# Kernel optimization log

Measured on AMD Instinct MI355X. Metric: run time of the kernel, lower is better.

## Reference

```python
import jax, jax.numpy as jnp
import numpy as np

B, S, D = 4, 4096, 1024

def setup_inputs() -> dict:
    key = jax.random.key(0)
    ks = jax.random.split(key, 8)
    scale = 1.0 / np.sqrt(D)
    return {
        "inputs": jax.random.normal(ks[0], (B, S, D), dtype=jnp.float32),
        "context": jax.random.normal(ks[1], (B, S, D), dtype=jnp.float32),
        "Wq": jax.random.normal(ks[2], (D, D), dtype=jnp.float32) * scale,
        "bq": jnp.zeros((D,), dtype=jnp.float32),
        "Wk": jax.random.normal(ks[3], (D, D), dtype=jnp.float32) * scale,
        "bk": jnp.zeros((D,), dtype=jnp.float32),
        "Wv": jax.random.normal(ks[4], (D, D), dtype=jnp.float32) * scale,
        "bv": jnp.zeros((D,), dtype=jnp.float32),
        "Wo": jax.random.normal(ks[5], (D, D), dtype=jnp.float32) * scale,
        "bo": jnp.zeros((D,), dtype=jnp.float32),
    }

def reference(inputs, context, Wq, bq, Wk, bk, Wv, bv, Wo, bo):
    phi = lambda x: jax.nn.elu(x) + 1.0
    q_phi = phi(jnp.einsum("bsd,de->bse", inputs, Wq) + bq)   # [B,S,D]
    k_phi = phi(jnp.einsum("bsd,de->bse", context, Wk) + bk)  # [B,S,D]
    v = jnp.einsum("bsd,de->bse", context, Wv) + bv           # [B,S,D]
    kv = jnp.einsum("bsd,bse->bde", k_phi, v)                 # [B,D,D]
    k_sum = jnp.sum(k_phi, axis=1)                            # [B,D]
    z = 1.0 / (jnp.einsum("bsd,bd->bs", q_phi, k_sum)[..., None] + 1e-6)  # [B,S,1]
    out = jnp.einsum("bsd,bde->bse", q_phi, kv) * z           # [B,S,D]
    return jnp.einsum("bsd,de->bse", out, Wo) + bo + inputs
```

## Files before the change

kernel.cpp:

```cpp
#include <hip/hip_runtime.h>


typedef __bf16 bf16x8 __attribute__((ext_vector_type(8)));
typedef __bf16 bf16x4 __attribute__((ext_vector_type(4)));
typedef float  f32x4  __attribute__((ext_vector_type(4)));

#define GLOBAL_AS __attribute__((address_space(1)))
#define LDS_AS    __attribute__((address_space(3)))

#define SS 4096
#define DD 1024

__device__ __forceinline__ __bf16 f2bf(float f) {
  union { float f; unsigned u; } a; a.f = f;
  unsigned r = a.u + 0x7FFFu + ((a.u >> 16) & 1u);
  union { unsigned short s; __bf16 b; } o; o.s = (unsigned short)(r >> 16);
  return o.b;
}

__device__ __forceinline__ void async_load16(const void* g, void* l) {
  __builtin_amdgcn_global_load_lds((const GLOBAL_AS void*)g, (LDS_AS void*)l, 16, 0, 0);
}


#define LA0 0
#define LA1 16384
#define LB0 32768
#define LB1 49152

#define VMW(n)  asm volatile("s_waitcnt vmcnt(" #n ")" ::: "memory")
#define SBAR()  asm volatile("s_barrier" ::: "memory")

#define STG_A(BASE, mh, kt) do {                                              \
    async_load16(Aa + (long)((mh)*64 + t6) * K + (kt)*64 + gc8,               \
                 smem + (BASE) + (mh)*8192 + tid*8);                          \
    async_load16(Aa + (long)(128 + (mh)*64 + t6) * K + (kt)*64 + gc8,         \
                 smem + (BASE) + (mh)*8192 + 4096 + tid*8);                   \
  } while (0)

#define STG_B(BASE, nh, kt) do {                                              \
    async_load16(Bb + (long)(tA*64 + (nh)*32 + t5) * K + (kt)*64 + gc8,       \
                 smem + (BASE) + (nh)*8192 + tid*8);                          \
    async_load16(Bb + (long)(128 + tA*64 + (nh)*32 + t5) * K + (kt)*64 + gc8, \
                 smem + (BASE) + (nh)*8192 + 4096 + tid*8);                   \
  } while (0)

#define RD_A(dst, AB, mh)                                                     \
    _Pragma("unroll") for (int rr = 0; rr < 4; ++rr) {                        \
      const int o = (AB) + (mh)*8192 + rr*1024 + aoff;                        \
      dst[rr][0] = *(const bf16x8*)(smem + o);                                \
      dst[rr][1] = *(const bf16x8*)(smem + (o ^ 32));                         \
    }

#define RD_B(dst, BB, nh)                                                     \
    _Pragma("unroll") for (int nn = 0; nn < 2; ++nn) {                        \
      const int o = (BB) + (nh)*8192 + nn*1024 + boff;                        \
      dst[nn][0] = *(const bf16x8*)(smem + o);                                \
      dst[nn][1] = *(const bf16x8*)(smem + (o ^ 32));                         \
    }

#define MM(mh, nh, af, bf)                                                    \
    __builtin_amdgcn_s_setprio(1);                                            \
    _Pragma("unroll") for (int rr = 0; rr < 4; ++rr)                          \
    _Pragma("unroll") for (int nn = 0; nn < 2; ++nn) {                        \
      acc[(mh)*4+rr][(nh)*2+nn] = __builtin_amdgcn_mfma_f32_16x16x32_bf16(    \
          af[rr][0], bf[nn][0], acc[(mh)*4+rr][(nh)*2+nn], 0, 0, 0);          \
      acc[(mh)*4+rr][(nh)*2+nn] = __builtin_amdgcn_mfma_f32_16x16x32_bf16(    \
          af[rr][1], bf[nn][1], acc[(mh)*4+rr][(nh)*2+nn], 0, 0, 0);          \
    }                                                                         \
    __builtin_amdgcn_s_setprio(0)

#define PH(VM, STG, RDS, MMM) do {                                            \
    VM; STG; RDS;                                                             \
    SBAR();                                                                   \
    MMM;                                                                      \
  } while (0)

template<int MODE>
__global__ __launch_bounds__(512, 2)
void gemm256(const __bf16* __restrict__ Ag, const __bf16* __restrict__ Bg,
             void* __restrict__ Cg, void* __restrict__ Cg2,
             int N, int K, long sB,
             const float* __restrict__ bias, const float* __restrict__ bias2,
             const float* __restrict__ zvec, const float* __restrict__ resid)
{
  union SMem {
    __bf16 st[65536];
    __bf16 T[256 * 136];
  };
  __shared__ SMem sm;
  __bf16* smem = sm.st;

  int bx = blockIdx.x, by = blockIdx.y;
  {
    const int gx = gridDim.x, gy = gridDim.y;
    if ((gy & 7) == 0) {
      const int f = by * gx + bx;
      const int j = f & 7;
      const int u = f >> 3;
      bx = u % gx;
      by = j * (gy >> 3) + u / gx;
    }
  }

  const int tid  = threadIdx.x;
  const int lane = tid & 63, wave = tid >> 6;
  const int wm   = wave >> 2, wn = wave & 3;
  const int ln   = lane & 15, quad = lane >> 4;
  const int t6   = tid >> 3, tA = t6 >> 5, t5 = t6 & 31;
  const int gc8  = ((tid & 7) ^ (t6 & 7)) * 8;
  const int pco  = (quad ^ (ln & 7)) * 8;
  const int aoff = (wm * 64 + ln) * 64 + pco;
  const int boff = (wn * 32 + ln) * 64 + pco;

  const long m0  = (long)by * 256;
  const int  n0g = bx * 256;
  const __bf16* Aa = Ag + m0 * K;
  const __bf16* Bb = Bg + (long)bx * 256 * K +
                     ((MODE == 8) ? (long)(m0 >> 12) * sB : 0);

  f32x4 acc[8][4];
  const f32x4 zero = {0.f, 0.f, 0.f, 0.f};
#pragma unroll
  for (int i = 0; i < 8; i++)
#pragma unroll
    for (int j = 0; j < 4; j++) acc[i][j] = zero;

  STG_A(LA0, 0, 0); STG_B(LB0, 0, 0);
  STG_A(LA0, 1, 0); STG_B(LB0, 1, 0);
  STG_A(LA1, 0, 1); STG_B(LB1, 0, 1);
  VMW(8);
  SBAR();

  const int niter = K >> 7;
#pragma unroll 1
  for (int i = 0; i < niter - 1; ++i) {
    const int kb = i * 2;
    bf16x8 a[4][2], b[2][2], b1[2][2];
    PH(VMW(4), STG_A(LA1,1,kb+1), RD_A(a,LA0,0) RD_B(b,LB0,0), MM(0,0,a,b));
    PH(      , STG_B(LB1,1,kb+1), RD_B(b1,LB0,1),              MM(0,1,a,b1));
    PH(      , STG_A(LA0,0,kb+2), RD_A(a,LA0,1),               MM(1,1,a,b1));
    PH(VMW(6), STG_B(LB0,0,kb+2), ,                            MM(1,0,a,b));
    PH(VMW(4), STG_A(LA0,1,kb+2), RD_A(a,LA1,0) RD_B(b,LB1,0), MM(0,0,a,b));
    PH(      , STG_B(LB0,1,kb+2), RD_B(b1,LB1,1),              MM(0,1,a,b1));
    PH(      , STG_A(LA1,0,kb+3), RD_A(a,LA1,1),               MM(1,1,a,b1));
    PH(VMW(6), STG_B(LB1,0,kb+3), ,                            MM(1,0,a,b));
  }
  {
    const int kb = (niter - 1) * 2;
    bf16x8 a[4][2], b[2][2], b1[2][2];
    PH(VMW(4), STG_A(LA1,1,kb+1), RD_A(a,LA0,0) RD_B(b,LB0,0), MM(0,0,a,b));
    PH(      , STG_B(LB1,1,kb+1), RD_B(b1,LB0,1),              MM(0,1,a,b1));
    PH(      , ,                  RD_A(a,LA0,1),               MM(1,1,a,b1));
    PH(VMW(0), ,                  ,                            MM(1,0,a,b));
    PH(      , ,                  RD_A(a,LA1,0) RD_B(b,LB1,0), MM(0,0,a,b));
    PH(      , ,                  RD_B(b1,LB1,1),              MM(0,1,a,b1));
    PH(      , ,                  RD_A(a,LA1,1),               MM(1,1,a,b1));
    PH(      , ,                  ,                            MM(1,0,a,b));
    SBAR();
  }

  if (MODE == 6) {
    const bool isK = (n0g < 1024);
    const float* bb = isK ? bias : bias2;
    const int nb = isK ? n0g : (n0g - 1024);
    const int b = (int)(m0 >> 12);
    const long s_in = m0 & 4095;
    __bf16* dst = (__bf16*)(isK ? Cg : Cg2) + (long)b * DD * SS;
#pragma unroll
    for (int h = 0; h < 2; ++h) {
      if (wm == h) {
#pragma unroll
        for (int mf = 0; mf < 8; ++mf)
#pragma unroll
          for (int nf = 0; nf < 4; ++nf) {
            const int nl = wn * 64 + nf * 16 + ln;
            const int sl0 = mf * 16 + quad * 4;
            const float bv = bb[nb + nl];
            bf16x4 pk;
#pragma unroll
            for (int r = 0; r < 4; ++r) {
              float x = acc[mf][nf][r] + bv;
              if (isK) x = (x > 0.f) ? (x + 1.f) : __expf(x);
              pk[r] = f2bf(x);
            }
            *(bf16x4*)(sm.T + nl * 136 + sl0) = pk;
          }
      }
      __syncthreads();
#pragma unroll
      for (int p2 = 0; p2 < 8; ++p2) {
        const int row = (tid >> 4) + p2 * 32;
        const int c   = (tid & 15) * 8;
        bf16x8 vv = *(const bf16x8*)(sm.T + row * 136 + c);
        *(bf16x8*)&dst[(long)(nb + row) * SS + s_in + h * 128 + c] = vv;
      }
      __syncthreads();
    }
    return;
  }

#pragma unroll
  for (int mf = 0; mf < 8; ++mf)
#pragma unroll
    for (int nf = 0; nf < 4; ++nf)
#pragma unroll
      for (int r = 0; r < 4; ++r) {
        const long gm = m0 + wm * 128 + mf * 16 + quad * 4 + r;
        const int  gn = n0g + wn * 64 + nf * 16 + ln;
        float x = acc[mf][nf][r];
        if (MODE == 0) {
          x += bias[gn];
          x = (x > 0.f) ? (x + 1.f) : __expf(x);
          ((__bf16*)Cg)[gm * (long)N + gn] = f2bf(x);
        } else {
          x = x * zvec[gm] + bias[gn];
          ((float*)Cg)[gm * (long)N + gn] = x + resid[gm * (long)N + gn];
        }
      }
}

#undef PH
#undef MM
#undef RD_A
#undef RD_B
#undef STG_A
#undef STG_B

template<int MODE>
__global__ __launch_bounds__(256)
void gemm_bt(const __bf16* __restrict__ Ag, const __bf16* __restrict__ Bg,
             void* __restrict__ Cg, void* __restrict__ Cg2,
             int N, int K, long sA, long sB, long sC,
             const float* __restrict__ bias, const float* __restrict__ bias2,
             const float* __restrict__ zvec,
             const float* __restrict__ resid)
{
  union SMem {
    struct { __bf16 As[128 * 64]; __bf16 Bs[128 * 64]; } s;
    __bf16 T[128 * 136];
  };
  __shared__ SMem sm;

  int bx = blockIdx.x, by = blockIdx.y;
  {
    const int gx = gridDim.x, gy = gridDim.y;
    if ((gy & 7) == 0) {
      const int f = by * gx + bx;
      const int j = f & 7;
      const int u = f >> 3;
      bx = u % gx;
      by = j * (gy >> 3) + u / gx;
    }
  }
  int bz = blockIdx.z;
  int k0beg = 0, k0end = K;
  if (MODE == 5) {
    const int split = bz & 3;
    bz >>= 2;
    k0beg = split * (K >> 2);
    k0end = k0beg + (K >> 2);
  }

  const int tid = threadIdx.x;
  const long m0 = (long)by * 128;
  const __bf16* A = Ag + m0 * K + bz * sA;
  const __bf16* B = Bg + (long)bx * 128 * K + bz * sB;

  const int srow = tid >> 3;
  const int gcc8 = ((tid & 7) ^ (srow & 7)) * 8;

  const int lane = tid & 63;
  const int wave = tid >> 6;
  const int wm   = (wave >> 1) * 64;
  const int wn   = (wave & 1) * 64;
  const int ln   = lane & 15;
  const int quad = lane >> 4;
  const int rk   = ln & 7;

  f32x4 acc[4][4];
  const f32x4 zero = {0.f, 0.f, 0.f, 0.f};
#pragma unroll
  for (int i = 0; i < 4; i++)
#pragma unroll
    for (int j = 0; j < 4; j++) acc[i][j] = zero;

  for (int k0 = k0beg; k0 < k0end; k0 += 64) {
#pragma unroll
    for (int p = 0; p < 4; p++) {
      async_load16(A + (long)(p * 32 + srow) * K + k0 + gcc8, sm.s.As + p * 2048 + tid * 8);
      async_load16(B + (long)(p * 32 + srow) * K + k0 + gcc8, sm.s.Bs + p * 2048 + tid * 8);
    }
    __syncthreads();

#pragma unroll
    for (int ksub = 0; ksub < 2; ksub++) {
      const int cc = (ksub * 4 + quad) ^ rk;
      bf16x8 af[4], bfr[4];
#pragma unroll
      for (int i = 0; i < 4; i++)
        af[i] = *(const bf16x8*)(sm.s.As + (wm + i * 16 + ln) * 64 + cc * 8);
#pragma unroll
      for (int j = 0; j < 4; j++)
        bfr[j] = *(const bf16x8*)(sm.s.Bs + (wn + j * 16 + ln) * 64 + cc * 8);
#pragma unroll
      for (int i = 0; i < 4; i++)
#pragma unroll
        for (int j = 0; j < 4; j++)
          acc[i][j] = __builtin_amdgcn_mfma_f32_16x16x32_bf16(af[i], bfr[j], acc[i][j], 0, 0, 0);
    }
    __syncthreads();
  }

  const int n0g = bx * 128;
#pragma unroll
  for (int i = 0; i < 4; i++) {
#pragma unroll
    for (int j = 0; j < 4; j++) {
#pragma unroll
      for (int r = 0; r < 4; r++) {
        const int lrow = wm + i * 16 + quad * 4 + r;
        const int lcol = wn + j * 16 + ln;
        const long gm  = m0 + lrow;
        const int  gn  = n0g + lcol;
        float x = acc[i][j][r];
        if (MODE == 5) {
          __hip_atomic_fetch_add(&((float*)Cg)[(long)bz * sC + gm * (long)N + gn],
                                 x, __ATOMIC_RELAXED, __HIP_MEMORY_SCOPE_AGENT);
        } else if (MODE == 7) {
          ((__bf16*)Cg)[(long)bz * sC + gm * (long)N + gn] = f2bf(x);
        }
      }
    }
  }
}

__global__ __launch_bounds__(256)
void cvt_f32_bf16(const float* __restrict__ x, __bf16* __restrict__ y, long n)
{
  long i = ((long)blockIdx.x * 256 + threadIdx.x) * 4;
  if (i < n) {
    float4 v = *(const float4*)(x + i);
    bf16x4 o;
    o[0] = f2bf(v.x); o[1] = f2bf(v.y); o[2] = f2bf(v.z); o[3] = f2bf(v.w);
    *(bf16x4*)(y + i) = o;
  }
}

__global__ __launch_bounds__(256)
void wtrans(const float* W0, const float* W1, const float* W2, const float* W3,
            __bf16* O0, __bf16* O1, __bf16* O2, __bf16* O3, int Dd)
{
  __shared__ __bf16 t[64][72];
  const float* W = (blockIdx.z == 0) ? W0 : (blockIdx.z == 1) ? W1 : (blockIdx.z == 2) ? W2 : W3;
  __bf16*      O = (blockIdx.z == 0) ? O0 : (blockIdx.z == 1) ? O1 : (blockIdx.z == 2) ? O2 : O3;
  const int r0 = blockIdx.y * 64, c0 = blockIdx.x * 64;
  const int tid = threadIdx.x;
  const int lr4 = tid >> 4, lc4 = (tid & 15) * 4;
#pragma unroll
  for (int it = 0; it < 4; it++) {
    const int row = lr4 + it * 16;
    float4 v = *(const float4*)&W[(long)(r0 + row) * Dd + c0 + lc4];
    t[row][lc4 + 0] = f2bf(v.x);
    t[row][lc4 + 1] = f2bf(v.y);
    t[row][lc4 + 2] = f2bf(v.z);
    t[row][lc4 + 3] = f2bf(v.w);
  }
  __syncthreads();
  const int lr8 = tid >> 3, lc8 = (tid & 7) * 8;
#pragma unroll
  for (int it = 0; it < 2; it++) {
    const int orow = lr8 + it * 32;
    bf16x8 vb;
#pragma unroll
    for (int j = 0; j < 8; j++) vb[j] = t[lc8 + j][orow];
    *(bf16x8*)&O[(long)(c0 + orow) * Dd + r0 + lc8] = vb;
  }
}

__global__ __launch_bounds__(256)
void ksum_k(const __bf16* __restrict__ kphiT, float* __restrict__ ksum, int S)
{
  const long row = blockIdx.x;
  const __bf16* p = kphiT + row * (long)S;
  const int tid = threadIdx.x;
  float s = 0.f;
  for (int j = tid * 8; j < S; j += 256 * 8) {
    bf16x8 v = *(const bf16x8*)&p[j];
#pragma unroll
    for (int e = 0; e < 8; e++) s += (float)v[e];
  }
  __shared__ float red[256];
  red[tid] = s; __syncthreads();
  for (int off = 128; off > 0; off >>= 1) {
    if (tid < off) red[tid] += red[tid + off];
    __syncthreads();
  }
  if (tid == 0) ksum[row] = red[0];
}

__global__ __launch_bounds__(256)
void zden_k(const __bf16* __restrict__ qphi, const float* __restrict__ ksum,
            float* __restrict__ z, int Dd, int S)
{
  const long row = blockIdx.x;
  const int  b   = (int)(row / S);
  const __bf16* q = qphi + row * (long)Dd;
  const float* ks = ksum + (long)b * Dd;
  const int tid = threadIdx.x;
  const int i = tid * 4;
  bf16x4 qv = *(const bf16x4*)&q[i];
  float4 kv4 = *(const float4*)&ks[i];
  float s = (float)qv[0] * kv4.x + (float)qv[1] * kv4.y +
            (float)qv[2] * kv4.z + (float)qv[3] * kv4.w;
  __shared__ float red[256];
  red[tid] = s; __syncthreads();
  for (int off = 128; off > 0; off >>= 1) {
    if (tid < off) red[tid] += red[tid + off];
    __syncthreads();
  }
  if (tid == 0) z[row] = 1.f / (red[0] + 1e-6f);
}

extern "C" void kernel_launch(void* const* d_in, const int* in_sizes, int n_in,
                              void* d_out, int out_size, void* d_ws, size_t ws_size,
                              hipStream_t stream)
{
  const float* inputs  = (const float*)d_in[0];
  const float* context = (const float*)d_in[1];
  const float* Wq = (const float*)d_in[2];
  const float* bq = (const float*)d_in[3];
  const float* Wk = (const float*)d_in[4];
  const float* bk = (const float*)d_in[5];
  const float* Wv = (const float*)d_in[6];
  const float* bv = (const float*)d_in[7];
  const float* Wo = (const float*)d_in[8];
  const float* bo = (const float*)d_in[9];
  float* out = (float*)d_out;

  const int Bn = 4;
  const long NSD = (long)Bn * SS * DD;
  const long MB = 1L << 20;

  char* ws = (char*)d_ws;
  __bf16* xbf   = (__bf16*)(ws + 0 * MB);
  __bf16* cbf   = (__bf16*)(ws + 32 * MB);
  __bf16* qphi  = (__bf16*)(ws + 64 * MB);
  __bf16* kphiT = (__bf16*)(ws + 96 * MB);
  __bf16* vT    = (__bf16*)(ws + 128 * MB);
  float*  kvf   = (float*)(ws + 160 * MB);
  __bf16* kvbf  = (__bf16*)(ws + 176 * MB);
  __bf16* M2T   = (__bf16*)(ws + 184 * MB);
  __bf16* WqT   = (__bf16*)(ws + 192 * MB);
  __bf16* WkT   = (__bf16*)(ws + 194 * MB);
  __bf16* WvT   = (__bf16*)(ws + 196 * MB);
  __bf16* WoT   = (__bf16*)(ws + 198 * MB);
  float*  ksum  = (float*)(ws + 200 * MB);
  float*  zbuf  = (float*)(ws + 201 * MB);

  cvt_f32_bf16<<<16384, 256, 0, stream>>>(inputs,  xbf, NSD);
  cvt_f32_bf16<<<16384, 256, 0, stream>>>(context, cbf, NSD);
  wtrans<<<dim3(16, 16, 4), 256, 0, stream>>>(Wq, Wk, Wv, Wo, WqT, WkT, WvT, WoT, DD);

  gemm256<0><<<dim3(4, 64), 512, 0, stream>>>(xbf, WqT, qphi, nullptr,
      DD, DD, 0, bq, nullptr, nullptr, nullptr);

  gemm256<6><<<dim3(8, 64), 512, 0, stream>>>(cbf, WkT, kphiT, vT,
      2048, DD, 0, bk, bv, nullptr, nullptr);

  ksum_k<<<4096, 256, 0, stream>>>(kphiT, ksum, SS);
  zden_k<<<16384, 256, 0, stream>>>(qphi, ksum, zbuf, DD, SS);

  hipMemsetAsync(kvf, 0, (size_t)Bn * DD * DD * sizeof(float), stream);
  gemm_bt<5><<<dim3(8, 8, 16), 256, 0, stream>>>(kphiT, vT, kvf, nullptr,
      DD, SS, (long)DD * SS, (long)DD * SS, (long)DD * DD,
      nullptr, nullptr, nullptr, nullptr);
  cvt_f32_bf16<<<4096, 256, 0, stream>>>(kvf, kvbf, (long)Bn * DD * DD);

  gemm_bt<7><<<dim3(8, 8, 4), 256, 0, stream>>>(WoT, kvbf, M2T, nullptr,
      DD, DD, 0, (long)DD * DD, (long)DD * DD, nullptr, nullptr, nullptr, nullptr);

  gemm256<8><<<dim3(4, 64), 512, 0, stream>>>(qphi, M2T, out, nullptr,
      DD, DD, (long)DD * DD, bo, nullptr, zbuf, inputs);
}
```

Before: 515.3 us.

## Move KV split-K GEMM to 256-tile kernel with partial buffers and reduce

The K^T·V product now runs on the larger 256x256 pipelined GEMM kernel with a 4-way split over the sequence. Each split writes its own fp32 partial buffer, replacing atomic adds into a memset-zeroed buffer. A new kernel sums the four partials and converts to bf16, replacing the separate conversion pass. The partial buffers reuse workspace freed by the earlier bf16 inputs, and the extra reduction reads four times the kv data.

Measured after the change: 462.8 us. 10.2% less time.

```diff
diff --git a/kernel.cpp b/kernel.cpp
--- a/kernel.cpp
+++ b/kernel.cpp
@@ -80,7 +80,7 @@
 __global__ __launch_bounds__(512, 2)
 void gemm256(const __bf16* __restrict__ Ag, const __bf16* __restrict__ Bg,
              void* __restrict__ Cg, void* __restrict__ Cg2,
-             int N, int K, long sB,
+             int N, int K, int Klen, long sA, long sB,
              const float* __restrict__ bias, const float* __restrict__ bias2,
              const float* __restrict__ zvec, const float* __restrict__ resid)
 {
@@ -92,7 +92,17 @@
   __bf16* smem = sm.st;
 
   int bx = blockIdx.x, by = blockIdx.y;
-  {
+  int zid = 0;
+  long koff = 0, abat = 0, bbat = 0;
+  if (MODE == 5) {
+    const int l = ((int)blockIdx.z * (int)gridDim.y + (int)blockIdx.y)
+                  * (int)gridDim.x + (int)blockIdx.x;
+    const int v = (l & 7) * 32 + (l >> 3);
+    bx = v & 3; by = (v >> 2) & 3; zid = v >> 4;
+    koff = (long)(zid & 3) * 1024;
+    abat = (long)(zid >> 2) * sA;
+    bbat = (long)(zid >> 2) * sB;
+  } else {
     const int gx = gridDim.x, gy = gridDim.y;
     if ((gy & 7) == 0) {
       const int f = by * gx + bx;
@@ -115,8 +125,8 @@
 
   const long m0  = (long)by * 256;
   const int  n0g = bx * 256;
-  const __bf16* Aa = Ag + m0 * K;
-  const __bf16* Bb = Bg + (long)bx * 256 * K +
+  const __bf16* Aa = Ag + m0 * K + koff + abat;
+  const __bf16* Bb = Bg + (long)bx * 256 * K + koff + bbat +
                      ((MODE == 8) ? (long)(m0 >> 12) * sB : 0);
 
   f32x4 acc[8][4];
@@ -132,7 +142,7 @@
   VMW(8);
   SBAR();
 
-  const int niter = K >> 7;
+  const int niter = Klen >> 7;
 #pragma unroll 1
   for (int i = 0; i < niter - 1; ++i) {
     const int kb = i * 2;
@@ -200,6 +210,7 @@
     return;
   }
 
+  const long zoff = (MODE == 5) ? (long)zid * DD * (long)DD : 0;
 #pragma unroll
   for (int mf = 0; mf < 8; ++mf)
 #pragma unroll
@@ -213,6 +224,8 @@
           x += bias[gn];
           x = (x > 0.f) ? (x + 1.f) : __expf(x);
           ((__bf16*)Cg)[gm * (long)N + gn] = f2bf(x);
+        } else if (MODE == 5) {
+          ((float*)Cg)[zoff + gm * (long)N + gn] = x;
         } else {
           x = x * zvec[gm] + bias[gn];
           ((float*)Cg)[gm * (long)N + gn] = x + resid[gm * (long)N + gn];
@@ -253,14 +266,7 @@
       by = j * (gy >> 3) + u / gx;
     }
   }
-  int bz = blockIdx.z;
-  int k0beg = 0, k0end = K;
-  if (MODE == 5) {
-    const int split = bz & 3;
-    bz >>= 2;
-    k0beg = split * (K >> 2);
-    k0end = k0beg + (K >> 2);
-  }
+  const int bz = blockIdx.z;
 
   const int tid = threadIdx.x;
   const long m0 = (long)by * 128;
@@ -285,7 +291,7 @@
 #pragma unroll
     for (int j = 0; j < 4; j++) acc[i][j] = zero;
 
-  for (int k0 = k0beg; k0 < k0end; k0 += 64) {
+  for (int k0 = 0; k0 < K; k0 += 64) {
 #pragma unroll
     for (int p = 0; p < 4; p++) {
       async_load16(A + (long)(p * 32 + srow) * K + k0 + gcc8, sm.s.As + p * 2048 + tid * 8);
@@ -323,12 +329,8 @@
         const int lcol = wn + j * 16 + ln;
         const long gm  = m0 + lrow;
         const int  gn  = n0g + lcol;
-        float x = acc[i][j][r];
-        if (MODE == 5) {
-          __hip_atomic_fetch_add(&((float*)Cg)[(long)bz * sC + gm * (long)N + gn],
-                                 x, __ATOMIC_RELAXED, __HIP_MEMORY_SCOPE_AGENT);
-        } else if (MODE == 7) {
-          ((__bf16*)Cg)[(long)bz * sC + gm * (long)N + gn] = f2bf(x);
+        if (MODE == 7) {
+          ((__bf16*)Cg)[(long)bz * sC + gm * (long)N + gn] = f2bf(acc[i][j][r]);
         }
       }
     }
@@ -345,6 +347,25 @@
     o[0] = f2bf(v.x); o[1] = f2bf(v.y); o[2] = f2bf(v.z); o[3] = f2bf(v.w);
     *(bf16x4*)(y + i) = o;
   }
+}
+
+__global__ __launch_bounds__(256)
+void reduce4_bf16(const float* __restrict__ kvf, __bf16* __restrict__ kvbf)
+{
+  const long g = (long)blockIdx.x * 256 + threadIdx.x;
+  const int  b = (int)(g >> 18);
+  const long i = (g & 262143L) * 4;
+  const float* p = kvf + (long)b * 4194304 + i;
+  float4 s0 = *(const float4*)(p);
+  float4 s1 = *(const float4*)(p + 1048576);
+  float4 s2 = *(const float4*)(p + 2097152);
+  float4 s3 = *(const float4*)(p + 3145728);
+  bf16x4 o;
+  o[0] = f2bf(s0.x + s1.x + s2.x + s3.x);
+  o[1] = f2bf(s0.y + s1.y + s2.y + s3.y);
+  o[2] = f2bf(s0.z + s1.z + s2.z + s3.z);
+  o[3] = f2bf(s0.w + s1.w + s2.w + s3.w);
+  *(bf16x4*)(kvbf + (long)b * 1048576 + i) = o;
 }
 
 __global__ __launch_bounds__(256)
@@ -445,10 +466,10 @@
   char* ws = (char*)d_ws;
   __bf16* xbf   = (__bf16*)(ws + 0 * MB);
   __bf16* cbf   = (__bf16*)(ws + 32 * MB);
+  float*  kvf   = (float*)(ws + 0 * MB);
   __bf16* qphi  = (__bf16*)(ws + 64 * MB);
   __bf16* kphiT = (__bf16*)(ws + 96 * MB);
   __bf16* vT    = (__bf16*)(ws + 128 * MB);
-  float*  kvf   = (float*)(ws + 160 * MB);
   __bf16* kvbf  = (__bf16*)(ws + 176 * MB);
   __bf16* M2T   = (__bf16*)(ws + 184 * MB);
   __bf16* WqT   = (__bf16*)(ws + 192 * MB);
@@ -463,23 +484,22 @@
   wtrans<<<dim3(16, 16, 4), 256, 0, stream>>>(Wq, Wk, Wv, Wo, WqT, WkT, WvT, WoT, DD);
 
   gemm256<0><<<dim3(4, 64), 512, 0, stream>>>(xbf, WqT, qphi, nullptr,
-      DD, DD, 0, bq, nullptr, nullptr, nullptr);
+      DD, DD, DD, 0, 0, bq, nullptr, nullptr, nullptr);
 
   gemm256<6><<<dim3(8, 64), 512, 0, stream>>>(cbf, WkT, kphiT, vT,
-      2048, DD, 0, bk, bv, nullptr, nullptr);
+      2048, DD, DD, 0, 0, bk, bv, nullptr, nullptr);
 
   ksum_k<<<4096, 256, 0, stream>>>(kphiT, ksum, SS);
   zden_k<<<16384, 256, 0, stream>>>(qphi, ksum, zbuf, DD, SS);
 
-  hipMemsetAsync(kvf, 0, (size_t)Bn * DD * DD * sizeof(float), stream);
-  gemm_bt<5><<<dim3(8, 8, 16), 256, 0, stream>>>(kphiT, vT, kvf, nullptr,
-      DD, SS, (long)DD * SS, (long)DD * SS, (long)DD * DD,
+  gemm256<5><<<dim3(4, 4, 16), 512, 0, stream>>>(kphiT, vT, kvf, nullptr,
+      DD, SS, DD, (long)DD * SS, (long)DD * SS,
       nullptr, nullptr, nullptr, nullptr);
-  cvt_f32_bf16<<<4096, 256, 0, stream>>>(kvf, kvbf, (long)Bn * DD * DD);
+  reduce4_bf16<<<4096, 256, 0, stream>>>(kvf, kvbf);
 
   gemm_bt<7><<<dim3(8, 8, 4), 256, 0, stream>>>(WoT, kvbf, M2T, nullptr,
       DD, DD, 0, (long)DD * DD, (long)DD * DD, nullptr, nullptr, nullptr, nullptr);
 
   gemm256<8><<<dim3(4, 64), 512, 0, stream>>>(qphi, M2T, out, nullptr,
-      DD, DD, (long)DD * DD, bo, nullptr, zbuf, inputs);
-}
+      DD, DD, DD, 0, (long)DD * DD, bo, nullptr, zbuf, inputs);
+}
```
